# Kernel tuning notes

Measured on AMD Instinct MI355X. Metric: run time of the kernel, lower is better.

## Reference

```python
import jax, jax.numpy as jnp
import numpy as np

D = 256    # lstm_encoder_size
B = 1024   # batch (number of agents/trajectories)
T = 512    # prediction horizon (recurrence steps)
EPS = 1e-5


def setup_inputs() -> dict:
    key = jax.random.key(0)
    k = jax.random.split(key, 10)
    s = 1.0 / np.sqrt(D)
    return {
        "KS_ALL": jax.random.normal(k[0], (1, B, D), jnp.float32),
        "next_vf": jax.random.normal(k[1], (B, T), jnp.float32),
        # Koopman operators (torch Linear stores [out, in]; no bias)
        "A_w": jax.random.normal(k[2], (D, D), jnp.float32) * (0.4 * s),  # contractive
        "B_w": jax.random.normal(k[3], (D, 1), jnp.float32) * s,
        # decoder params (liner_dec=False)
        "W0": jax.random.normal(k[4], (2 * D, D), jnp.float32) * s,
        "b0": jnp.zeros((2 * D,), jnp.float32),
        "W1": jax.random.normal(k[5], (D, 2 * D), jnp.float32) / np.sqrt(2.0 * D),
        "b1": jnp.zeros((D,), jnp.float32),
        "ln_g": jnp.ones((D,), jnp.float32),
        "ln_b": jnp.zeros((D,), jnp.float32),
        "W2": jax.random.normal(k[6], (D, D), jnp.float32) * s,
        "b2": jnp.zeros((D,), jnp.float32),
        "W3": jax.random.normal(k[7], (3, D), jnp.float32) * s,
        "b3": jnp.zeros((3,), jnp.float32),
    }


def _layer_norm(x, g, b):
    mu = jnp.mean(x, axis=-1, keepdims=True)
    var = jnp.var(x, axis=-1, keepdims=True)
    return (x - mu) * jax.lax.rsqrt(var + EPS) * g + b


def reference(KS_ALL, next_vf, A_w, B_w, W0, b0, W1, b1, ln_g, ln_b, W2, b2, W3, b3):
    # train_flag=True -> use only the first time slice of KS_ALL
    ks0 = KS_ALL[0]                 # [B, D]
    u = next_vf.T                   # [T, B] time-major, matches permute(1,0,2)
    b_vec = B_w[:, 0]               # [D]  (Linear(1, D) on scalar input)

    def step(ks, u_t):
        ks_new = ks @ A_w.T + u_t[:, None] * b_vec[None, :]  # [B, D]
        return ks_new, ks_new

    _, ks_seq = jax.lax.scan(step, ks0, u)                   # [T, B, D]
    KS_pre = jnp.concatenate([ks0[None], ks_seq], axis=0)    # [T+1, B, D]

    # nonlinear decoder (eval mode: dropout is identity; use_elu=True)
    s1 = jnp.tanh(KS_pre @ W0.T + b0)          # [T+1, B, 2D]
    s2 = jnp.tanh(s1 @ W1.T + b1)              # [T+1, B, D]
    s2 = _layer_norm(KS_pre + s2, ln_g, ln_b)  # AddAndNorm
    s3 = jax.nn.elu(s2 @ W2.T + b2)
    OS = s3 @ W3.T + b3                        # [T+1, B, 3]
    return KS_pre, OS
```

## Files before the change

kernel.cpp:

```cpp
#include <hip/hip_runtime.h>

typedef unsigned short u16;
typedef __attribute__((ext_vector_type(8))) short bf16x8;
typedef __attribute__((ext_vector_type(4))) short bf16x4;
typedef __attribute__((ext_vector_type(4))) float f32x4;

#define MFMA16(a, b, c) __builtin_amdgcn_mfma_f32_16x16x32_bf16((a), (b), (c), 0, 0, 0)

#define OFF_UPAD 0
#define OFF_KS0  589824
#define OFF_W0   851968
#define OFF_W1   983040
#define OFF_W2   1114112
#define OFF_CRT  1179648
#define OFF_P    1196032
#define OS_OFF   134479872

__device__ __forceinline__ u16 f2bf(float f) {
  union { float f; unsigned int i; } v; v.f = f;
  return (u16)((v.i + 0x7fffu + ((v.i >> 16) & 1u)) >> 16);
}
__device__ __forceinline__ float bf2f(u16 u) {
  union { unsigned int i; float f; } v; v.i = ((unsigned int)u) << 16;
  return v.f;
}
__device__ __forceinline__ float fast_tanh(float x) {
  float e = __expf(2.0f * x);
  return 1.0f - __fdividef(2.0f, e + 1.0f);
}

__global__ void k_prep(const float* __restrict__ KS_ALL, const float* __restrict__ next_vf,
                       const float* __restrict__ A_w, const float* __restrict__ W0,
                       const float* __restrict__ W1, const float* __restrict__ W2,
                       u16* __restrict__ ws) {
  int idx = blockIdx.x * 256 + threadIdx.x;
  if (idx < 589824) {
    int r = idx / 576, c = idx % 576;
    ws[OFF_UPAD + idx] = (c < 64) ? (u16)0 : f2bf(next_vf[r * 512 + c - 64]);
    return;
  }
  idx -= 589824;
  if (idx < 262144) { ws[OFF_KS0 + idx] = f2bf(KS_ALL[idx]); return; }
  idx -= 262144;
  if (idx < 131072) { ws[OFF_W0 + idx] = f2bf(W0[idx]); return; }
  idx -= 131072;
  if (idx < 131072) { ws[OFF_W1 + idx] = f2bf(W1[idx]); return; }
  idx -= 131072;
  if (idx < 65536)  { ws[OFF_W2 + idx] = f2bf(W2[idx]); return; }
  idx -= 65536;
  if (idx < 65536) {
    int r = idx >> 8, c = idx & 255;
    ws[OFF_P + idx] = (r == c) ? (u16)0x3F80 : (u16)0;
    ws[OFF_P + 65536 + idx] = f2bf(A_w[idx]);
  }
}

__global__ __launch_bounds__(512) void k_pow(u16* __restrict__ ws, int s) {
  const u16* P = ws + OFF_P;
  int j = blockIdx.y + 1;
  int mh = blockIdx.x;
  int lane = threadIdx.x & 63, w = threadIdx.x >> 6;
  int wm = w >> 2, wn = w & 3;
  int lg = lane >> 4, ll = lane & 15;
  const u16* Am = P + s * 65536;
  const u16* Bm = P + j * 65536;
  f32x4 acc[4][4];
  f32x4 z = {0.f, 0.f, 0.f, 0.f};
#pragma unroll
  for (int mi = 0; mi < 4; ++mi)
#pragma unroll
    for (int ni = 0; ni < 4; ++ni) acc[mi][ni] = z;
#pragma unroll
  for (int ks = 0; ks < 8; ++ks) {
    bf16x8 a[4], b[4];
    int kk = ks * 32 + lg * 8;
#pragma unroll
    for (int mi = 0; mi < 4; ++mi) {
      int row = mh * 128 + wm * 64 + mi * 16 + ll;
      a[mi] = *(const bf16x8*)(Am + row * 256 + kk);
    }
#pragma unroll
    for (int ni = 0; ni < 4; ++ni) {
      int col = wn * 64 + ni * 16 + ll;
#pragma unroll
      for (int e = 0; e < 8; ++e) b[ni][e] = (short)Bm[(kk + e) * 256 + col];
    }
#pragma unroll
    for (int mi = 0; mi < 4; ++mi)
#pragma unroll
      for (int ni = 0; ni < 4; ++ni) acc[mi][ni] = MFMA16(a[mi], b[ni], acc[mi][ni]);
  }
  u16* Pd = ws + OFF_P + (s + j) * 65536;
#pragma unroll
  for (int mi = 0; mi < 4; ++mi)
#pragma unroll
    for (int ni = 0; ni < 4; ++ni)
#pragma unroll
      for (int r = 0; r < 4; ++r) {
        int row = mh * 128 + wm * 64 + mi * 16 + lg * 4 + r;
        int col = wn * 64 + ni * 16 + ll;
        Pd[row * 256 + col] = f2bf(acc[mi][ni][r]);
      }
}

__global__ void k_crevt(const float* __restrict__ B_w, u16* __restrict__ ws) {
  int s = blockIdx.x;
  int n = threadIdx.x;
  const u16* Pr = ws + OFF_P + (63 - s) * 65536 + n * 256;
  float acc = 0.f;
  for (int k = 0; k < 256; ++k) acc += bf2f(Pr[k]) * B_w[k];
  ws[OFF_CRT + n * 64 + s] = f2bf(acc);
}

__global__ __launch_bounds__(512, 1) void k_fused(
    const u16* __restrict__ ws,
    const float* __restrict__ b0, const float* __restrict__ b1,
    const float* __restrict__ lng, const float* __restrict__ lnb,
    const float* __restrict__ b2, const float* __restrict__ W3,
    const float* __restrict__ b3, float* __restrict__ out) {
  __shared__ __align__(16) u16 Xb[16384];
  __shared__ __align__(16) unsigned char Hraw[66560];
  __shared__ float par[2308];
  u16* Hb = (u16*)Hraw;
  float* Hf = (float*)Hraw;

  float* pb0 = par;
  float* pb1 = par + 512;
  float* pg  = par + 768;
  float* pbt = par + 1024;
  float* pb2 = par + 1280;
  float* pW3 = par + 1536;
  float* pb3 = par + 2304;

  const int t  = blockIdx.y;
  const int R0 = blockIdx.x * 64;
  const int tid = threadIdx.x;
  const int lane = tid & 63, w = tid >> 6;
  const int lg = lane >> 4, ll = lane & 15;

  pb0[tid] = b0[tid];
  if (tid < 256) { pb1[tid] = b1[tid]; pg[tid] = lng[tid]; pbt[tid] = lnb[tid]; pb2[tid] = b2[tid]; }
  pW3[tid < 512 ? tid : 0] = W3[tid < 512 ? tid : 0];
  if (tid < 256) pW3[512 + tid] = W3[512 + tid];
  if (tid < 4) pb3[tid] = (tid < 3) ? b3[tid] : 0.f;

  {
    const u16* src = ws + OFF_CRT;
#pragma unroll
    for (int c = 0; c < 4; ++c) {
      int cid = c * 512 + tid;
      int n = cid >> 3, q = cid & 7;
      bf16x8 v = *(const bf16x8*)(src + n * 64 + q * 8);
      int byt = ((n << 7) + (q << 4)) ^ ((n & 7) << 4);
      *(bf16x8*)(Hb + (byt >> 1)) = v;
    }
  }
  __syncthreads();

  f32x4 z = {0.f, 0.f, 0.f, 0.f};

  f32x4 acc[4][2];
#pragma unroll
  for (int mi = 0; mi < 4; ++mi)
#pragma unroll
    for (int ni = 0; ni < 2; ++ni) acc[mi][ni] = z;
  {
    bf16x8 au[4][2];
#pragma unroll
    for (int mi = 0; mi < 4; ++mi)
#pragma unroll
      for (int ksu = 0; ksu < 2; ++ksu) {
        const u16* up = ws + OFF_UPAD + (R0 + mi * 16 + ll) * 576 + t + ksu * 32 + lg * 8;
#pragma unroll
        for (int e = 0; e < 8; ++e) au[mi][ksu][e] = (short)up[e];
      }
#pragma unroll
    for (int ksu = 0; ksu < 2; ++ksu)
#pragma unroll
      for (int ni = 0; ni < 2; ++ni) {
        int n = w * 32 + ni * 16 + ll;
        int byt = ((n << 7) + ksu * 64 + (lg << 4)) ^ ((n & 7) << 4);
        bf16x8 bfr = *(const bf16x8*)(Hb + (byt >> 1));
#pragma unroll
        for (int mi = 0; mi < 4; ++mi) acc[mi][ni] = MFMA16(au[mi][ksu], bfr, acc[mi][ni]);
      }
    if (t < 64) {
      const u16* Pt = ws + OFF_P + t * 65536;
      const u16* ks0b = ws + OFF_KS0;
#pragma unroll
      for (int ks = 0; ks < 8; ++ks) {
        bf16x8 a[4], b[2];
#pragma unroll
        for (int mi = 0; mi < 4; ++mi)
          a[mi] = *(const bf16x8*)(ks0b + (R0 + mi * 16 + ll) * 256 + ks * 32 + lg * 8);
#pragma unroll
        for (int ni = 0; ni < 2; ++ni)
          b[ni] = *(const bf16x8*)(Pt + (w * 32 + ni * 16 + ll) * 256 + ks * 32 + lg * 8);
#pragma unroll
        for (int mi = 0; mi < 4; ++mi)
#pragma unroll
          for (int ni = 0; ni < 2; ++ni) acc[mi][ni] = MFMA16(a[mi], b[ni], acc[mi][ni]);
      }
    }
  }
  __syncthreads();

#pragma unroll
  for (int mi = 0; mi < 4; ++mi)
#pragma unroll
    for (int ni = 0; ni < 2; ++ni)
#pragma unroll
      for (int r = 0; r < 4; ++r)
        Hf[(mi * 16 + lg * 4 + r) * 260 + w * 32 + ni * 16 + ll] = acc[mi][ni][r];
  __syncthreads();

  {
    float* ob = out + (size_t)t * 262144 + (size_t)R0 * 256;
#pragma unroll
    for (int it = 0; it < 8; ++it) {
      int idx = it * 512 + tid;
      int row = idx >> 6, c4 = idx & 63;
      f32x4 v = *(const f32x4*)(Hf + row * 260 + c4 * 4);
      __builtin_nontemporal_store(v, (f32x4*)(ob + row * 256 + c4 * 4));
      bf16x4 h;
#pragma unroll
      for (int e = 0; e < 4; ++e) h[e] = (short)f2bf(v[e]);
      int byt = (((row << 9) + ((c4 >> 1) << 4)) ^ ((row & 7) << 4)) + ((c4 & 1) << 3);
      *(bf16x4*)(Xb + (byt >> 1)) = h;
    }
  }
  __syncthreads();

  const u16* W0b = ws + OFF_W0;
#pragma unroll 1
  for (int h = 0; h < 2; ++h) {
#pragma unroll
    for (int mi = 0; mi < 4; ++mi)
#pragma unroll
      for (int ni = 0; ni < 2; ++ni) acc[mi][ni] = z;
#pragma unroll
    for (int ks = 0; ks < 8; ++ks) {
      bf16x8 a[4], b[2];
#pragma unroll
      for (int mi = 0; mi < 4; ++mi) {
        int rl = mi * 16 + ll;
        int byt = ((rl << 9) + ks * 64 + (lg << 4)) ^ ((rl & 7) << 4);
        a[mi] = *(const bf16x8*)(Xb + (byt >> 1));
      }
#pragma unroll
      for (int ni = 0; ni < 2; ++ni) {
        int n = h * 256 + w * 32 + ni * 16 + ll;
        b[ni] = *(const bf16x8*)(W0b + n * 256 + ks * 32 + lg * 8);
      }
#pragma unroll
      for (int mi = 0; mi < 4; ++mi)
#pragma unroll
        for (int ni = 0; ni < 2; ++ni) acc[mi][ni] = MFMA16(a[mi], b[ni], acc[mi][ni]);
    }
#pragma unroll
    for (int mi = 0; mi < 4; ++mi)
#pragma unroll
      for (int ni = 0; ni < 2; ++ni)
#pragma unroll
        for (int r = 0; r < 4; ++r) {
          int rl = mi * 16 + lg * 4 + r;
          int col = h * 256 + w * 32 + ni * 16 + ll;
          float v = fast_tanh(acc[mi][ni][r] + pb0[col]);
          int byt = ((rl << 10) + (col << 1)) ^ ((rl & 7) << 4);
          Hb[byt >> 1] = f2bf(v);
        }
  }
  __syncthreads();

#pragma unroll
  for (int mi = 0; mi < 4; ++mi)
#pragma unroll
    for (int ni = 0; ni < 2; ++ni) acc[mi][ni] = z;
  {
    const u16* W1b = ws + OFF_W1;
#pragma unroll
    for (int ks = 0; ks < 16; ++ks) {
      bf16x8 a[4], b[2];
#pragma unroll
      for (int mi = 0; mi < 4; ++mi) {
        int rl = mi * 16 + ll;
        int byt = ((rl << 10) + ks * 64 + (lg << 4)) ^ ((rl & 7) << 4);
        a[mi] = *(const bf16x8*)(Hb + (byt >> 1));
      }
#pragma unroll
      for (int ni = 0; ni < 2; ++ni) {
        int n = w * 32 + ni * 16 + ll;
        b[ni] = *(const bf16x8*)(W1b + n * 512 + ks * 32 + lg * 8);
      }
#pragma unroll
      for (int mi = 0; mi < 4; ++mi)
#pragma unroll
        for (int ni = 0; ni < 2; ++ni) acc[mi][ni] = MFMA16(a[mi], b[ni], acc[mi][ni]);
    }
  }
  __syncthreads();

#pragma unroll
  for (int mi = 0; mi < 4; ++mi)
#pragma unroll
    for (int ni = 0; ni < 2; ++ni)
#pragma unroll
      for (int r = 0; r < 4; ++r) {
        int rl = mi * 16 + lg * 4 + r;
        int col = w * 32 + ni * 16 + ll;
        float v = fast_tanh(acc[mi][ni][r] + pb1[col]);
        int bx = ((rl << 9) + (col << 1)) ^ ((rl & 7) << 4);
        v += bf2f(Xb[bx >> 1]);
        Hb[rl * 256 + col] = f2bf(v);
      }
  __syncthreads();

  {
    int row = tid >> 3, jq = tid & 7;
    const u16* hr = Hb + row * 256 + jq * 32;
    bf16x8 chv[4];
#pragma unroll
    for (int q = 0; q < 4; ++q) chv[q] = *(const bf16x8*)(hr + q * 8);
    float s = 0.f, ss = 0.f;
#pragma unroll
    for (int q = 0; q < 4; ++q)
#pragma unroll
      for (int e = 0; e < 8; ++e) { float v = bf2f((u16)chv[q][e]); s += v; ss += v * v; }
    s += __shfl_xor(s, 1);  s += __shfl_xor(s, 2);  s += __shfl_xor(s, 4);
    ss += __shfl_xor(ss, 1); ss += __shfl_xor(ss, 2); ss += __shfl_xor(ss, 4);
    float mu = s * 0.00390625f;
    float var = ss * 0.00390625f - mu * mu;
    float rstd = rsqrtf(var + 1e-5f);
#pragma unroll
    for (int q = 0; q < 4; ++q) {
      bf16x8 o;
#pragma unroll
      for (int e = 0; e < 8; ++e) {
        int col = jq * 32 + q * 8 + e;
        float v = (bf2f((u16)chv[q][e]) - mu) * rstd * pg[col] + pbt[col];
        o[e] = (short)f2bf(v);
      }
      int byt = ((row << 9) + ((jq * 32 + q * 8) << 1)) ^ ((row & 7) << 4);
      *(bf16x8*)(Hb + (byt >> 1)) = o;
    }
  }
  __syncthreads();

#pragma unroll
  for (int mi = 0; mi < 4; ++mi)
#pragma unroll
    for (int ni = 0; ni < 2; ++ni) acc[mi][ni] = z;
  {
    const u16* W2b = ws + OFF_W2;
#pragma unroll
    for (int ks = 0; ks < 8; ++ks) {
      bf16x8 a[4], b[2];
#pragma unroll
      for (int mi = 0; mi < 4; ++mi) {
        int rl = mi * 16 + ll;
        int byt = ((rl << 9) + ks * 64 + (lg << 4)) ^ ((rl & 7) << 4);
        a[mi] = *(const bf16x8*)(Hb + (byt >> 1));
      }
#pragma unroll
      for (int ni = 0; ni < 2; ++ni) {
        int n = w * 32 + ni * 16 + ll;
        b[ni] = *(const bf16x8*)(W2b + n * 256 + ks * 32 + lg * 8);
      }
#pragma unroll
      for (int mi = 0; mi < 4; ++mi)
#pragma unroll
        for (int ni = 0; ni < 2; ++ni) acc[mi][ni] = MFMA16(a[mi], b[ni], acc[mi][ni]);
    }
  }
#pragma unroll
  for (int mi = 0; mi < 4; ++mi)
#pragma unroll
    for (int ni = 0; ni < 2; ++ni)
#pragma unroll
      for (int r = 0; r < 4; ++r) {
        int rl = mi * 16 + lg * 4 + r;
        int col = w * 32 + ni * 16 + ll;
        float v = acc[mi][ni][r] + pb2[col];
        v = v > 0.f ? v : (__expf(v) - 1.f);
        Xb[rl * 256 + col] = f2bf(v);
      }
  __syncthreads();

  {
    int row = tid >> 3, jq = tid & 7;
    const u16* xr = Xb + row * 256 + jq * 32;
    float d0 = 0.f, d1 = 0.f, d2 = 0.f;
#pragma unroll
    for (int q = 0; q < 4; ++q) {
      bf16x8 c = *(const bf16x8*)(xr + q * 8);
#pragma unroll
      for (int e = 0; e < 8; ++e) {
        float v = bf2f((u16)c[e]);
        int col = jq * 32 + q * 8 + e;
        d0 += v * pW3[col]; d1 += v * pW3[256 + col]; d2 += v * pW3[512 + col];
      }
    }
    d0 += __shfl_xor(d0, 1); d0 += __shfl_xor(d0, 2); d0 += __shfl_xor(d0, 4);
    d1 += __shfl_xor(d1, 1); d1 += __shfl_xor(d1, 2); d1 += __shfl_xor(d1, 4);
    d2 += __shfl_xor(d2, 1); d2 += __shfl_xor(d2, 2); d2 += __shfl_xor(d2, 4);
    if (jq == 0) {
      int grow = R0 + row;
      int ob = OS_OFF + t * 3072 + grow * 3;
      out[ob]     = d0 + pb3[0];
      out[ob + 1] = d1 + pb3[1];
      out[ob + 2] = d2 + pb3[2];
    }
  }
}

extern "C" void kernel_launch(void* const* d_in, const int* in_sizes, int n_in,
                              void* d_out, int out_size, void* d_ws, size_t ws_size,
                              hipStream_t stream) {
  const float* KS_ALL  = (const float*)d_in[0];
  const float* next_vf = (const float*)d_in[1];
  const float* A_w     = (const float*)d_in[2];
  const float* B_w     = (const float*)d_in[3];
  const float* W0      = (const float*)d_in[4];
  const float* b0      = (const float*)d_in[5];
  const float* W1      = (const float*)d_in[6];
  const float* b1      = (const float*)d_in[7];
  const float* lng     = (const float*)d_in[8];
  const float* lnb     = (const float*)d_in[9];
  const float* W2      = (const float*)d_in[10];
  const float* b2      = (const float*)d_in[11];
  const float* W3      = (const float*)d_in[12];
  const float* b3      = (const float*)d_in[13];
  u16* ws = (u16*)d_ws;
  float* out = (float*)d_out;

  k_prep<<<4864, 256, 0, stream>>>(KS_ALL, next_vf, A_w, W0, W1, W2, ws);
  for (int s = 1; s <= 32; s <<= 1)
    k_pow<<<dim3(2, s), 512, 0, stream>>>(ws, s);
  k_crevt<<<64, 256, 0, stream>>>(B_w, ws);
  k_fused<<<dim3(16, 513), 512, 0, stream>>>(ws, b0, b1, lng, lnb, b2, W3, b3, out);
}
```

Baseline: 1.500 ms.

## Cut LDS footprint by chunking layer-1/2 GEMMs and staging output in halves

Shrinks shared memory per block by splitting the layer-1 output into two 256-column halves, each immediately consumed by a partial layer-2 GEMM that accumulates into a separate register accumulator. The fp32 KS output staging is done in two 32-row passes so the buffer fits in the smaller region. Launch bounds are raised to allow more resident blocks per CU, and later LDS tiles switch from XOR swizzle to a padded 264 stride. Streaming stores become regular stores. The extra accumulator set raises register pressure, which may conflict with the higher occupancy target and could cause spills, and the extra barriers add synchronisation.

```diff
diff --git a/kernel.cpp b/kernel.cpp
--- a/kernel.cpp
+++ b/kernel.cpp
@@ -112,14 +112,14 @@
   ws[OFF_CRT + n * 64 + s] = f2bf(acc);
 }
 
-__global__ __launch_bounds__(512, 1) void k_fused(
+__global__ __launch_bounds__(512, 4) void k_fused(
     const u16* __restrict__ ws,
     const float* __restrict__ b0, const float* __restrict__ b1,
     const float* __restrict__ lng, const float* __restrict__ lnb,
     const float* __restrict__ b2, const float* __restrict__ W3,
     const float* __restrict__ b3, float* __restrict__ out) {
-  __shared__ __align__(16) u16 Xb[16384];
-  __shared__ __align__(16) unsigned char Hraw[66560];
+  __shared__ __align__(16) u16 Xb[16896];
+  __shared__ __align__(16) unsigned char Hraw[33792];
   __shared__ float par[2308];
   u16* Hb = (u16*)Hraw;
   float* Hf = (float*)Hraw;
@@ -140,7 +140,7 @@
 
   pb0[tid] = b0[tid];
   if (tid < 256) { pb1[tid] = b1[tid]; pg[tid] = lng[tid]; pbt[tid] = lnb[tid]; pb2[tid] = b2[tid]; }
-  pW3[tid < 512 ? tid : 0] = W3[tid < 512 ? tid : 0];
+  if (tid < 512) pW3[tid] = W3[tid];
   if (tid < 256) pW3[512 + tid] = W3[512 + tid];
   if (tid < 4) pb3[tid] = (tid < 3) ? b3[tid] : 0.f;
 
@@ -205,33 +205,43 @@
   }
   __syncthreads();
 
-#pragma unroll
-  for (int mi = 0; mi < 4; ++mi)
-#pragma unroll
-    for (int ni = 0; ni < 2; ++ni)
-#pragma unroll
-      for (int r = 0; r < 4; ++r)
-        Hf[(mi * 16 + lg * 4 + r) * 260 + w * 32 + ni * 16 + ll] = acc[mi][ni][r];
-  __syncthreads();
-
-  {
-    float* ob = out + (size_t)t * 262144 + (size_t)R0 * 256;
-#pragma unroll
-    for (int it = 0; it < 8; ++it) {
+#pragma unroll 1
+  for (int p = 0; p < 2; ++p) {
+#pragma unroll
+    for (int mi2 = 0; mi2 < 2; ++mi2) {
+      int mi = p * 2 + mi2;
+#pragma unroll
+      for (int ni = 0; ni < 2; ++ni)
+#pragma unroll
+        for (int r = 0; r < 4; ++r)
+          Hf[(mi2 * 16 + lg * 4 + r) * 260 + w * 32 + ni * 16 + ll] = acc[mi][ni][r];
+    }
+    __syncthreads();
+    float* ob = out + (size_t)t * 262144 + (size_t)(R0 + p * 32) * 256;
+#pragma unroll
+    for (int it = 0; it < 4; ++it) {
       int idx = it * 512 + tid;
       int row = idx >> 6, c4 = idx & 63;
       f32x4 v = *(const f32x4*)(Hf + row * 260 + c4 * 4);
-      __builtin_nontemporal_store(v, (f32x4*)(ob + row * 256 + c4 * 4));
+      *(f32x4*)(ob + row * 256 + c4 * 4) = v;
+      int rl = p * 32 + row;
       bf16x4 h;
 #pragma unroll
       for (int e = 0; e < 4; ++e) h[e] = (short)f2bf(v[e]);
-      int byt = (((row << 9) + ((c4 >> 1) << 4)) ^ ((row & 7) << 4)) + ((c4 & 1) << 3);
+      int byt = (((rl << 9) + ((c4 >> 1) << 4)) ^ ((rl & 7) << 4)) + ((c4 & 1) << 3);
       *(bf16x4*)(Xb + (byt >> 1)) = h;
     }
-  }
-  __syncthreads();
+    __syncthreads();
+  }
 
   const u16* W0b = ws + OFF_W0;
+  const u16* W1b = ws + OFF_W1;
+  f32x4 accL2[4][2];
+#pragma unroll
+  for (int mi = 0; mi < 4; ++mi)
+#pragma unroll
+    for (int ni = 0; ni < 2; ++ni) accL2[mi][ni] = z;
+
 #pragma unroll 1
   for (int h = 0; h < 2; ++h) {
 #pragma unroll
@@ -264,41 +274,33 @@
 #pragma unroll
         for (int r = 0; r < 4; ++r) {
           int rl = mi * 16 + lg * 4 + r;
-          int col = h * 256 + w * 32 + ni * 16 + ll;
-          float v = fast_tanh(acc[mi][ni][r] + pb0[col]);
-          int byt = ((rl << 10) + (col << 1)) ^ ((rl & 7) << 4);
+          int col_l = w * 32 + ni * 16 + ll;
+          float v = fast_tanh(acc[mi][ni][r] + pb0[h * 256 + col_l]);
+          int byt = ((rl << 9) + (col_l << 1)) ^ ((rl & 7) << 4);
           Hb[byt >> 1] = f2bf(v);
         }
-  }
-  __syncthreads();
-
-#pragma unroll
-  for (int mi = 0; mi < 4; ++mi)
-#pragma unroll
-    for (int ni = 0; ni < 2; ++ni) acc[mi][ni] = z;
-  {
-    const u16* W1b = ws + OFF_W1;
-#pragma unroll
-    for (int ks = 0; ks < 16; ++ks) {
+    __syncthreads();
+#pragma unroll
+    for (int ks = 0; ks < 8; ++ks) {
       bf16x8 a[4], b[2];
 #pragma unroll
       for (int mi = 0; mi < 4; ++mi) {
         int rl = mi * 16 + ll;
-        int byt = ((rl << 10) + ks * 64 + (lg << 4)) ^ ((rl & 7) << 4);
+        int byt = ((rl << 9) + ks * 64 + (lg << 4)) ^ ((rl & 7) << 4);
         a[mi] = *(const bf16x8*)(Hb + (byt >> 1));
       }
 #pragma unroll
       for (int ni = 0; ni < 2; ++ni) {
         int n = w * 32 + ni * 16 + ll;
-        b[ni] = *(const bf16x8*)(W1b + n * 512 + ks * 32 + lg * 8);
+        b[ni] = *(const bf16x8*)(W1b + n * 512 + h * 256 + ks * 32 + lg * 8);
       }
 #pragma unroll
       for (int mi = 0; mi < 4; ++mi)
 #pragma unroll
-        for (int ni = 0; ni < 2; ++ni) acc[mi][ni] = MFMA16(a[mi], b[ni], acc[mi][ni]);
-    }
-  }
-  __syncthreads();
+        for (int ni = 0; ni < 2; ++ni) accL2[mi][ni] = MFMA16(a[mi], b[ni], accL2[mi][ni]);
+    }
+    __syncthreads();
+  }
 
 #pragma unroll
   for (int mi = 0; mi < 4; ++mi)
@@ -308,16 +310,16 @@
       for (int r = 0; r < 4; ++r) {
         int rl = mi * 16 + lg * 4 + r;
         int col = w * 32 + ni * 16 + ll;
-        float v = fast_tanh(acc[mi][ni][r] + pb1[col]);
+        float v = fast_tanh(accL2[mi][ni][r] + pb1[col]);
         int bx = ((rl << 9) + (col << 1)) ^ ((rl & 7) << 4);
         v += bf2f(Xb[bx >> 1]);
-        Hb[rl * 256 + col] = f2bf(v);
+        Hb[rl * 264 + col] = f2bf(v);
       }
   __syncthreads();
 
   {
     int row = tid >> 3, jq = tid & 7;
-    const u16* hr = Hb + row * 256 + jq * 32;
+    u16* hr = Hb + row * 264 + jq * 32;
     bf16x8 chv[4];
 #pragma unroll
     for (int q = 0; q < 4; ++q) chv[q] = *(const bf16x8*)(hr + q * 8);
@@ -340,8 +342,7 @@
         float v = (bf2f((u16)chv[q][e]) - mu) * rstd * pg[col] + pbt[col];
         o[e] = (short)f2bf(v);
       }
-      int byt = ((row << 9) + ((jq * 32 + q * 8) << 1)) ^ ((row & 7) << 4);
-      *(bf16x8*)(Hb + (byt >> 1)) = o;
+      *(bf16x8*)(hr + q * 8) = o;
     }
   }
   __syncthreads();
@@ -358,8 +359,7 @@
 #pragma unroll
       for (int mi = 0; mi < 4; ++mi) {
         int rl = mi * 16 + ll;
-        int byt = ((rl << 9) + ks * 64 + (lg << 4)) ^ ((rl & 7) << 4);
-        a[mi] = *(const bf16x8*)(Hb + (byt >> 1));
+        a[mi] = *(const bf16x8*)(Hb + rl * 264 + ks * 32 + lg * 8);
       }
 #pragma unroll
       for (int ni = 0; ni < 2; ++ni) {
@@ -382,13 +382,13 @@
         int col = w * 32 + ni * 16 + ll;
         float v = acc[mi][ni][r] + pb2[col];
         v = v > 0.f ? v : (__expf(v) - 1.f);
-        Xb[rl * 256 + col] = f2bf(v);
+        Xb[rl * 264 + col] = f2bf(v);
       }
   __syncthreads();
 
   {
     int row = tid >> 3, jq = tid & 7;
-    const u16* xr = Xb + row * 256 + jq * 32;
+    const u16* xr = Xb + row * 264 + jq * 32;
     float d0 = 0.f, d1 = 0.f, d2 = 0.f;
 #pragma unroll
     for (int q = 0; q < 4; ++q) {
```

New measurement: 1.955 ms. 1.3x slower.
